# Kernel optimization log

Measured on AMD Instinct MI355X. Metric: run time of the kernel, lower is better.

The kernel has to match this reference:

```python
import jax, jax.numpy as jnp
import numpy as np

# opts hyperparameters (SCAN defaults)
LAMBDA_SOFTMAX = 9.0   # opts.lambda_softmax
LAMBDA_LSE = 6.0       # opts.lambda_lse
MARGIN = 0.2           # ContrastiveLoss margin
MAX_VIOLATION = False
NEG_INF = -1e9


def setup_inputs() -> dict:
    key = jax.random.key(0)
    k1, k2, k3 = jax.random.split(key, 3)
    I, C, R, W, D = 96, 96, 36, 48, 256  # n_image, n_recipe, n_region, max_words, dim
    images = jax.random.normal(k1, (I, R, D), dtype=jnp.float32)
    recipes = jax.random.normal(k2, (C, W, D), dtype=jnp.float32)
    # valid caption lengths in [8, W] so every caption has real words
    cap_lens = jax.random.randint(k3, (C,), 8, W + 1).astype(jnp.int32)
    return {"images": images, "recipes": recipes, "cap_lens": cap_lens}


def _xattn_score_i2t(images, recipes, cap_lens):
    """Vectorized (masked) version of the per-caption python loop.
    images: (I, R, D), recipes: (C, W, D), cap_lens: (C,) -> scores (I, C)."""
    C, W, _ = recipes.shape
    valid = jnp.arange(W)[None, :] < cap_lens[:, None]          # (C, W)
    vm = valid[:, None, :, None]                                 # (C,1,W,1)

    # raw attention: context=words (query of bmm), query=regions -> (C, I, W, R)
    attn = jnp.einsum('cwd,ird->ciwr', recipes, images)
    # clipped_l2norm: leaky_relu then l2-normalize over the word dim (dim=1 of (I,W,R))
    attn = jax.nn.leaky_relu(attn, 0.1) * vm
    nrm = jnp.sqrt(jnp.sum(attn * attn, axis=2, keepdims=True))
    attn = attn / jnp.maximum(nrm, 1e-12)

    # softmax over words with temperature lambda_softmax, masked to valid words
    logits = jnp.where(vm, attn * LAMBDA_SOFTMAX, NEG_INF)
    aw = jax.nn.softmax(logits, axis=2)                          # (C, I, W, R)

    # weighted word context per region: (C, I, R, D)
    wctx = jnp.einsum('ciwr,cwd->cird', aw, recipes)

    # cosine similarity between image regions and their attended word context
    num = jnp.einsum('cird,ird->cir', wctx, images)              # (C, I, R)
    n1 = jnp.linalg.norm(images, axis=-1)                        # (I, R)
    n2 = jnp.linalg.norm(wctx, axis=-1)                          # (C, I, R)
    row_sim = num / jnp.maximum(n1[None] * n2, 1e-8)

    # LogSumExp aggregation over regions
    sim = jax.scipy.special.logsumexp(LAMBDA_LSE * row_sim, axis=-1) / LAMBDA_LSE  # (C, I)
    return sim.T                                                  # (I, C)


def reference(images, recipes, cap_lens):
    scores = _xattn_score_i2t(images, recipes, cap_lens)          # (I, C), I == C
    B = scores.shape[0]
    diag = jnp.diagonal(scores)                                   # (B,)
    eye = jnp.eye(B, dtype=bool)
    # d2[i,j] = diag[j] (positive image score), d1[i,j] = diag[i]
    cost_image = jnp.where(eye, 0.0, jnp.maximum(MARGIN + scores - diag[None, :], 0.0))
    cost_recipe = jnp.where(eye, 0.0, jnp.maximum(MARGIN + scores - diag[:, None], 0.0))
    if MAX_VIOLATION:
        cost_image = cost_image.max(axis=0)
        cost_recipe = cost_recipe.max(axis=1)
    return cost_image.sum() + cost_recipe.sum()
```

## Files before the change

kernel.cpp:

```cpp
#include <hip/hip_runtime.h>
#include <math.h>

#define I_N 96
#define C_N 96
#define R_N 36
#define W_N 48
#define D_N 256
#define NIMG 4
#define NCOL (NIMG * R_N)
#define LAM_SM 9.0f
#define LAM_LSE 6.0f
#define MARGIN_F 0.2f
#define AWS 56

#define IMG_ELEMS (I_N * R_N * D_N)
#define REC_ELEMS (C_N * W_N * D_N)

#define WSF_SCORES 0
#define WSF_N1     9216
#define WSF_SHBASE 12800
#define SH_IMG 0
#define SH_REC IMG_ELEMS
#define SH_GP  (IMG_ELEMS + REC_ELEMS)

typedef __attribute__((ext_vector_type(8))) short short8;
typedef __attribute__((ext_vector_type(4))) float f32x4;

#define MFMA16(a, b, c) __builtin_amdgcn_mfma_f32_16x16x32_bf16(a, b, c, 0, 0, 0)

__device__ __forceinline__ unsigned short f32_to_bf16(float f) {
    unsigned int u = __float_as_uint(f);
    return (unsigned short)((u + 0x7fffu + ((u >> 16) & 1u)) >> 16);
}
__device__ __forceinline__ float dot4f(float4 a, float4 b) {
    return a.x * b.x + a.y * b.y + a.z * b.z + a.w * b.w;
}
__device__ __forceinline__ uint4 cvt8u(float4 v0, float4 v1) {
    uint4 o;
    o.x = (unsigned)f32_to_bf16(v0.x) | ((unsigned)f32_to_bf16(v0.y) << 16);
    o.y = (unsigned)f32_to_bf16(v0.z) | ((unsigned)f32_to_bf16(v0.w) << 16);
    o.z = (unsigned)f32_to_bf16(v1.x) | ((unsigned)f32_to_bf16(v1.y) << 16);
    o.w = (unsigned)f32_to_bf16(v1.z) | ((unsigned)f32_to_bf16(v1.w) << 16);
    return o;
}
__device__ __forceinline__ short8 cvt8s(float4 v0, float4 v1) {
    short8 s;
    s[0] = (short)f32_to_bf16(v0.x); s[1] = (short)f32_to_bf16(v0.y);
    s[2] = (short)f32_to_bf16(v0.z); s[3] = (short)f32_to_bf16(v0.w);
    s[4] = (short)f32_to_bf16(v1.x); s[5] = (short)f32_to_bf16(v1.y);
    s[6] = (short)f32_to_bf16(v1.z); s[7] = (short)f32_to_bf16(v1.w);
    return s;
}

__global__ __launch_bounds__(256) void prep_all(
    const float* __restrict__ images, const float* __restrict__ recipes,
    unsigned short* __restrict__ img_p, unsigned short* __restrict__ rec_p,
    unsigned short* __restrict__ Gp, float* __restrict__ n1sq)
{
    __shared__ unsigned short gt[4 * 48 * 56];
    const int bid = blockIdx.x;
    const int t = threadIdx.x;
    const int wv = t >> 6, l = t & 63;
    const int li = l & 15, q = l >> 4;

    if (bid < 72) {
        const int tile = bid / 3, chunk = bid % 3;
        const float* src = images + (size_t)tile * NCOL * D_N;
        unsigned short* dst = img_p + (size_t)tile * 72 * 512;
        #pragma unroll
        for (int ff = 0; ff < 6; ++ff) {
            int f = chunk * 24 + wv * 6 + ff;
            int rg = f >> 3, ks = f & 7;
            const float* p = src + (rg * 16 + li) * D_N + ks * 32 + q * 8;
            *(uint4*)(dst + (size_t)f * 512 + l * 8) =
                cvt8u(*(const float4*)p, *(const float4*)(p + 4));
        }
    } else if (bid < 96) {
        const int c = (bid - 72) * 4 + wv;
        const float* src = recipes + (size_t)c * W_N * D_N;
        unsigned short* rdst = rec_p + (size_t)c * 24 * 512;
        f32x4 acc[3][3];
        #pragma unroll
        for (int m = 0; m < 3; ++m)
            #pragma unroll
            for (int j = 0; j < 3; ++j) acc[m][j] = (f32x4){0.f, 0.f, 0.f, 0.f};
        #pragma unroll
        for (int ks = 0; ks < 8; ++ks) {
            short8 a[3];
            #pragma unroll
            for (int m = 0; m < 3; ++m) {
                const float* p = src + (m * 16 + li) * D_N + ks * 32 + q * 8;
                a[m] = cvt8s(*(const float4*)p, *(const float4*)(p + 4));
                *(short8*)(rdst + ((size_t)m * 8 + ks) * 512 + l * 8) = a[m];
            }
            #pragma unroll
            for (int m = 0; m < 3; ++m)
                #pragma unroll
                for (int j = 0; j < 3; ++j)
                    acc[m][j] = MFMA16(a[m], a[j], acc[m][j]);
        }
        unsigned short* g = gt + wv * 48 * 56;
        #pragma unroll
        for (int m = 0; m < 3; ++m)
            #pragma unroll
            for (int j = 0; j < 3; ++j)
                #pragma unroll
                for (int r = 0; r < 4; ++r)
                    g[(16 * m + 4 * q + r) * 56 + 16 * j + li] =
                        f32_to_bf16(acc[m][j][r]);
        asm volatile("s_waitcnt lgkmcnt(0)" ::: "memory");
        __builtin_amdgcn_sched_barrier(0);
        unsigned short* dst = Gp + (size_t)c * 3072;
        #pragma unroll
        for (int m = 0; m < 3; ++m)
            #pragma unroll
            for (int ks = 0; ks < 2; ++ks) {
                union { short8 s; uint4 u; } v;
                v.u = make_uint4(0u, 0u, 0u, 0u);
                if (32 * ks + 8 * q < 48)
                    v.s = *(const short8*)(g + (16 * m + li) * 56 + 32 * ks + 8 * q);
                *(short8*)(dst + (m * 2 + ks) * 512 + l * 8) = v.s;
            }
    } else {
        const int row = (bid - 96) * 64 + (t >> 2);
        const int sub = t & 3;
        if (row < I_N * R_N) {
            const float4* p = (const float4*)(images + (size_t)row * D_N + sub * 64);
            float s = 0.f;
            #pragma unroll
            for (int k = 0; k < 16; ++k) { float4 v = p[k]; s += dot4f(v, v); }
            s += __shfl_xor(s, 1);
            s += __shfl_xor(s, 2);
            if (sub == 0) n1sq[row] = s;
        }
    }
}

__global__ __launch_bounds__(192, 4) void xattn_main(
    const unsigned short* __restrict__ img_p, const unsigned short* __restrict__ rec_p,
    const unsigned short* __restrict__ Gp, const int* __restrict__ cap_lens,
    const float* __restrict__ n1sq, float* __restrict__ scores)
{
    __shared__ __align__(16) unsigned short ldsA[24 * 512];
    __shared__ float rs[NCOL];
    unsigned short* awL = ldsA;

    const int t = threadIdx.x;
    const int wv = t >> 6;
    const int l = t & 63;
    const int li = l & 15, q = l >> 4;
    const int sbid = ((blockIdx.x & 7) * 288) + (blockIdx.x >> 3);
    const int c = sbid % C_N;
    const int T = sbid / C_N;
    const int L = cap_lens[c];
    const int n0 = wv * 48;

    const unsigned short* pB = img_p + ((size_t)T * 72 + wv * 24) * 512 + l * 8;
    short8 bA[2][3], bB[2][3];

    #pragma unroll
    for (int kk = 0; kk < 2; ++kk)
        #pragma unroll
        for (int j = 0; j < 3; ++j)
            bA[kk][j] = *(const short8*)(pB + (j * 8 + kk) * 512);

    {
        const unsigned short* pA = rec_p + (size_t)c * 24 * 512 + l * 8;
        #pragma unroll
        for (int f0 = 0; f0 < 8; ++f0) {
            int f = wv * 8 + f0;
            *(short8*)(ldsA + f * 512 + l * 8) = *(const short8*)(pA + f * 512);
        }
    }
    __syncthreads();

    f32x4 acc[3][3];
    #pragma unroll
    for (int m = 0; m < 3; ++m)
        #pragma unroll
        for (int j = 0; j < 3; ++j) acc[m][j] = (f32x4){0.f, 0.f, 0.f, 0.f};

    #pragma unroll
    for (int kk = 0; kk < 2; ++kk)
        #pragma unroll
        for (int j = 0; j < 3; ++j)
            bB[kk][j] = *(const short8*)(pB + (j * 8 + 2 + kk) * 512);
    #pragma unroll
    for (int kk = 0; kk < 2; ++kk) {
        short8 a[3];
        #pragma unroll
        for (int m = 0; m < 3; ++m)
            a[m] = *(const short8*)(ldsA + (m * 8 + kk) * 512 + l * 8);
        #pragma unroll
        for (int m = 0; m < 3; ++m)
            #pragma unroll
            for (int j = 0; j < 3; ++j)
                acc[m][j] = MFMA16(a[m], bA[kk][j], acc[m][j]);
    }
    #pragma unroll
    for (int kk = 0; kk < 2; ++kk)
        #pragma unroll
        for (int j = 0; j < 3; ++j)
            bA[kk][j] = *(const short8*)(pB + (j * 8 + 4 + kk) * 512);
    #pragma unroll
    for (int kk = 0; kk < 2; ++kk) {
        short8 a[3];
        #pragma unroll
        for (int m = 0; m < 3; ++m)
            a[m] = *(const short8*)(ldsA + (m * 8 + 2 + kk) * 512 + l * 8);
        #pragma unroll
        for (int m = 0; m < 3; ++m)
            #pragma unroll
            for (int j = 0; j < 3; ++j)
                acc[m][j] = MFMA16(a[m], bB[kk][j], acc[m][j]);
    }
    #pragma unroll
    for (int kk = 0; kk < 2; ++kk)
        #pragma unroll
        for (int j = 0; j < 3; ++j)
            bB[kk][j] = *(const short8*)(pB + (j * 8 + 6 + kk) * 512);
    #pragma unroll
    for (int kk = 0; kk < 2; ++kk) {
        short8 a[3];
        #pragma unroll
        for (int m = 0; m < 3; ++m)
            a[m] = *(const short8*)(ldsA + (m * 8 + 4 + kk) * 512 + l * 8);
        #pragma unroll
        for (int m = 0; m < 3; ++m)
            #pragma unroll
            for (int j = 0; j < 3; ++j)
                acc[m][j] = MFMA16(a[m], bA[kk][j], acc[m][j]);
    }
    #pragma unroll
    for (int kk = 0; kk < 2; ++kk) {
        short8 a[3];
        #pragma unroll
        for (int m = 0; m < 3; ++m)
            a[m] = *(const short8*)(ldsA + (m * 8 + 6 + kk) * 512 + l * 8);
        #pragma unroll
        for (int m = 0; m < 3; ++m)
            #pragma unroll
            for (int j = 0; j < 3; ++j)
                acc[m][j] = MFMA16(a[m], bB[kk][j], acc[m][j]);
    }
    __syncthreads();

    short8 gA[3][2];
    {
        const unsigned short* pg = Gp + (size_t)c * 3072 + l * 8;
        #pragma unroll
        for (int m = 0; m < 3; ++m)
            #pragma unroll
            for (int ks = 0; ks < 2; ++ks)
                gA[m][ks] = *(const short8*)(pg + (m * 2 + ks) * 512);
    }
    float n1v[3];
    #pragma unroll
    for (int j = 0; j < 3; ++j)
        n1v[j] = n1sq[T * NCOL + n0 + 16 * j + li];

    float nume[3];
    #pragma unroll
    for (int j = 0; j < 3; ++j) {
        const int n = n0 + 16 * j + li;
        float v[3][4];
        float ssq = 0.f;
        #pragma unroll
        for (int m = 0; m < 3; ++m)
            #pragma unroll
            for (int r = 0; r < 4; ++r) {
                int w = 16 * m + 4 * q + r;
                float x = acc[m][j][r];
                float lv = fmaxf(x, 0.1f * x);
                float lm = (w < L) ? lv : 0.f;
                v[m][r] = lm;
                ssq = fmaf(lm, lm, ssq);
            }
        ssq += __shfl_xor(ssq, 16); ssq += __shfl_xor(ssq, 32);
        float inv = LAM_SM * rsqrtf(fmaxf(ssq, 1e-24f));
        float np = 0.f;
        #pragma unroll
        for (int m = 0; m < 3; ++m) {
            int w0 = 16 * m + 4 * q;
            float e0 = (w0     < L) ? __expf(v[m][0] * inv) : 0.f;
            float e1 = (w0 + 1 < L) ? __expf(v[m][1] * inv) : 0.f;
            float e2 = (w0 + 2 < L) ? __expf(v[m][2] * inv) : 0.f;
            float e3 = (w0 + 3 < L) ? __expf(v[m][3] * inv) : 0.f;
            np = fmaf(e0, acc[m][j][0], np);
            np = fmaf(e1, acc[m][j][1], np);
            np = fmaf(e2, acc[m][j][2], np);
            np = fmaf(e3, acc[m][j][3], np);
            unsigned lo, hi;
            asm("v_cvt_pk_bf16_f32 %0, %1, %2" : "=v"(lo) : "v"(e0), "v"(e1));
            asm("v_cvt_pk_bf16_f32 %0, %1, %2" : "=v"(hi) : "v"(e2), "v"(e3));
            *(uint2*)(awL + n * AWS + 16 * m + 4 * q) = make_uint2(lo, hi);
        }
        np += __shfl_xor(np, 16); np += __shfl_xor(np, 32);
        nume[j] = np;
    }
    asm volatile("s_waitcnt lgkmcnt(0)" ::: "memory");
    __builtin_amdgcn_sched_barrier(0);

    #pragma unroll
    for (int m = 0; m < 3; ++m)
        #pragma unroll
        for (int j = 0; j < 3; ++j) acc[m][j] = (f32x4){0.f, 0.f, 0.f, 0.f};
    #pragma unroll
    for (int ks = 0; ks < 2; ++ks) {
        short8 b[3];
        #pragma unroll
        for (int j = 0; j < 3; ++j) {
            union { short8 s; uint4 u; } bv;
            bv.u = make_uint4(0u, 0u, 0u, 0u);
            if (32 * ks + 8 * q < 48) {
                const uint2* p =
                    (const uint2*)(awL + (n0 + 16 * j + li) * AWS + 32 * ks + 8 * q);
                uint2 x0 = p[0], x1 = p[1];
                bv.u = make_uint4(x0.x, x0.y, x1.x, x1.y);
            }
            b[j] = bv.s;
        }
        #pragma unroll
        for (int m = 0; m < 3; ++m)
            #pragma unroll
            for (int j = 0; j < 3; ++j)
                acc[m][j] = MFMA16(gA[m][ks], b[j], acc[m][j]);
    }

    #pragma unroll
    for (int j = 0; j < 3; ++j) {
        const int n = n0 + 16 * j + li;
        const unsigned short* ap = awL + n * AWS + 4 * q;
        float n2p = 0.f;
        #pragma unroll
        for (int m = 0; m < 3; ++m) {
            uint2 u = *(const uint2*)(ap + 16 * m);
            n2p = fmaf(__uint_as_float(u.x << 16),          acc[m][j][0], n2p);
            n2p = fmaf(__uint_as_float(u.x & 0xffff0000u),  acc[m][j][1], n2p);
            n2p = fmaf(__uint_as_float(u.y << 16),          acc[m][j][2], n2p);
            n2p = fmaf(__uint_as_float(u.y & 0xffff0000u),  acc[m][j][3], n2p);
        }
        n2p += __shfl_xor(n2p, 16); n2p += __shfl_xor(n2p, 32);
        if (q == 0)
            rs[n] = nume[j] * rsqrtf(fmaxf(n1v[j] * n2p, 1e-16f));
    }
    __syncthreads();

    if (t < 32) {
        int ii = t >> 3, k = t & 7;
        float mx = -1e30f;
        #pragma unroll
        for (int p = 0; p < 5; ++p) {
            int r = k + 8 * p;
            if (r < R_N) mx = fmaxf(mx, rs[ii * R_N + r]);
        }
        mx = fmaxf(mx, __shfl_xor(mx, 1));
        mx = fmaxf(mx, __shfl_xor(mx, 2));
        mx = fmaxf(mx, __shfl_xor(mx, 4));
        float s = 0.f;
        #pragma unroll
        for (int p = 0; p < 5; ++p) {
            int r = k + 8 * p;
            if (r < R_N) s += __expf(LAM_LSE * (rs[ii * R_N + r] - mx));
        }
        s += __shfl_xor(s, 1); s += __shfl_xor(s, 2); s += __shfl_xor(s, 4);
        if (k == 0)
            scores[(size_t)(T * NIMG + ii) * C_N + c] =
                (LAM_LSE * mx + __logf(s)) / LAM_LSE;
    }
}

__global__ __launch_bounds__(1024) void hinge_loss_kernel(
    const float* __restrict__ S, float* __restrict__ out)
{
    __shared__ float diag[96];
    __shared__ float wsum[16];
    const int t = threadIdx.x;
    if (t < 96) diag[t] = S[t * 97];
    __syncthreads();
    float acc = 0.f;
    #pragma unroll
    for (int p = 0; p < 9; ++p) {
        int k = t + 1024 * p;
        if (k < C_N * C_N) {
            int ii = k / 96;
            int cc = k - ii * 96;
            if (ii != cc) {
                float s = S[k];
                acc += fmaxf(MARGIN_F + s - diag[cc], 0.f)
                     + fmaxf(MARGIN_F + s - diag[ii], 0.f);
            }
        }
    }
    #pragma unroll
    for (int off = 32; off; off >>= 1) acc += __shfl_xor(acc, off);
    if ((t & 63) == 0) wsum[t >> 6] = acc;
    __syncthreads();
    if (t == 0) {
        float s = 0.f;
        #pragma unroll
        for (int w = 0; w < 16; ++w) s += wsum[w];
        out[0] = s;
    }
}

extern "C" void kernel_launch(void* const* d_in, const int* in_sizes, int n_in,
                              void* d_out, int out_size, void* d_ws, size_t ws_size,
                              hipStream_t stream) {
    const float* images  = (const float*)d_in[0];
    const float* recipes = (const float*)d_in[1];
    const int*   caps    = (const int*)d_in[2];
    float* out = (float*)d_out;
    float* wsf = (float*)d_ws;
    float* scores = wsf + WSF_SCORES;
    float* n1 = wsf + WSF_N1;
    unsigned short* shb = (unsigned short*)(wsf + WSF_SHBASE);
    unsigned short* img_p = shb + SH_IMG;
    unsigned short* rec_p = shb + SH_REC;
    unsigned short* Gpp   = shb + SH_GP;

    hipLaunchKernelGGL(prep_all, dim3(150), dim3(256), 0, stream,
                       images, recipes, img_p, rec_p, Gpp, n1);
    hipLaunchKernelGGL(xattn_main, dim3(2304), dim3(192), 0, stream,
                       img_p, rec_p, Gpp, caps, n1, scores);
    hipLaunchKernelGGL(hinge_loss_kernel, dim3(1), dim3(1024), 0, stream, scores, out);
}
```

Measured before the change: 39.03 us.

## Process three image tiles per block, reusing recipe LDS and softmax-context operands

Each block of xattn_main now loops over three image tiles for a given caption, so the grid shrinks from 2304 to 768 blocks. The recipe tile is loaded into LDS once, along with the G operand registers, and reused across the three tiles. A separate LDS buffer holds the attention weights, so the next tile's image fragments can be prefetched while the current tile's softmax runs. In exchange it uses more LDS per block, lowers the occupancy hint from 4 to 3, serializes work within a block, and leaves fewer blocks to spread across the CUs.

```diff
diff --git a/kernel.cpp b/kernel.cpp
--- a/kernel.cpp
+++ b/kernel.cpp
@@ -136,115 +136,44 @@
     }
 }
 
-__global__ __launch_bounds__(192, 4) void xattn_main(
+__global__ __launch_bounds__(192, 3) void xattn_main(
     const unsigned short* __restrict__ img_p, const unsigned short* __restrict__ rec_p,
     const unsigned short* __restrict__ Gp, const int* __restrict__ cap_lens,
     const float* __restrict__ n1sq, float* __restrict__ scores)
 {
-    __shared__ __align__(16) unsigned short ldsA[24 * 512];
+    __shared__ __align__(16) unsigned short recL[24 * 512];
+    __shared__ __align__(16) unsigned short awL[NCOL * AWS];
     __shared__ float rs[NCOL];
-    unsigned short* awL = ldsA;
 
     const int t = threadIdx.x;
     const int wv = t >> 6;
     const int l = t & 63;
     const int li = l & 15, q = l >> 4;
-    const int sbid = ((blockIdx.x & 7) * 288) + (blockIdx.x >> 3);
+    const int sbid = ((blockIdx.x & 7) * 96) + (blockIdx.x >> 3);
     const int c = sbid % C_N;
-    const int T = sbid / C_N;
+    const int tg = sbid / C_N;
     const int L = cap_lens[c];
     const int n0 = wv * 48;
 
-    const unsigned short* pB = img_p + ((size_t)T * 72 + wv * 24) * 512 + l * 8;
     short8 bA[2][3], bB[2][3];
 
-    #pragma unroll
-    for (int kk = 0; kk < 2; ++kk)
-        #pragma unroll
-        for (int j = 0; j < 3; ++j)
-            bA[kk][j] = *(const short8*)(pB + (j * 8 + kk) * 512);
-
+    {
+        const unsigned short* pB0 =
+            img_p + ((size_t)(3 * tg) * 72 + wv * 24) * 512 + l * 8;
+        #pragma unroll
+        for (int kk = 0; kk < 2; ++kk)
+            #pragma unroll
+            for (int j = 0; j < 3; ++j)
+                bA[kk][j] = *(const short8*)(pB0 + (j * 8 + kk) * 512);
+    }
     {
         const unsigned short* pA = rec_p + (size_t)c * 24 * 512 + l * 8;
         #pragma unroll
         for (int f0 = 0; f0 < 8; ++f0) {
             int f = wv * 8 + f0;
-            *(short8*)(ldsA + f * 512 + l * 8) = *(const short8*)(pA + f * 512);
-        }
-    }
-    __syncthreads();
-
-    f32x4 acc[3][3];
-    #pragma unroll
-    for (int m = 0; m < 3; ++m)
-        #pragma unroll
-        for (int j = 0; j < 3; ++j) acc[m][j] = (f32x4){0.f, 0.f, 0.f, 0.f};
-
-    #pragma unroll
-    for (int kk = 0; kk < 2; ++kk)
-        #pragma unroll
-        for (int j = 0; j < 3; ++j)
-            bB[kk][j] = *(const short8*)(pB + (j * 8 + 2 + kk) * 512);
-    #pragma unroll
-    for (int kk = 0; kk < 2; ++kk) {
-        short8 a[3];
-        #pragma unroll
-        for (int m = 0; m < 3; ++m)
-            a[m] = *(const short8*)(ldsA + (m * 8 + kk) * 512 + l * 8);
-        #pragma unroll
-        for (int m = 0; m < 3; ++m)
-            #pragma unroll
-            for (int j = 0; j < 3; ++j)
-                acc[m][j] = MFMA16(a[m], bA[kk][j], acc[m][j]);
-    }
-    #pragma unroll
-    for (int kk = 0; kk < 2; ++kk)
-        #pragma unroll
-        for (int j = 0; j < 3; ++j)
-            bA[kk][j] = *(const short8*)(pB + (j * 8 + 4 + kk) * 512);
-    #pragma unroll
-    for (int kk = 0; kk < 2; ++kk) {
-        short8 a[3];
-        #pragma unroll
-        for (int m = 0; m < 3; ++m)
-            a[m] = *(const short8*)(ldsA + (m * 8 + 2 + kk) * 512 + l * 8);
-        #pragma unroll
-        for (int m = 0; m < 3; ++m)
-            #pragma unroll
-            for (int j = 0; j < 3; ++j)
-                acc[m][j] = MFMA16(a[m], bB[kk][j], acc[m][j]);
-    }
-    #pragma unroll
-    for (int kk = 0; kk < 2; ++kk)
-        #pragma unroll
-        for (int j = 0; j < 3; ++j)
-            bB[kk][j] = *(const short8*)(pB + (j * 8 + 6 + kk) * 512);
-    #pragma unroll
-    for (int kk = 0; kk < 2; ++kk) {
-        short8 a[3];
-        #pragma unroll
-        for (int m = 0; m < 3; ++m)
-            a[m] = *(const short8*)(ldsA + (m * 8 + 4 + kk) * 512 + l * 8);
-        #pragma unroll
-        for (int m = 0; m < 3; ++m)
-            #pragma unroll
-            for (int j = 0; j < 3; ++j)
-                acc[m][j] = MFMA16(a[m], bA[kk][j], acc[m][j]);
-    }
-    #pragma unroll
-    for (int kk = 0; kk < 2; ++kk) {
-        short8 a[3];
-        #pragma unroll
-        for (int m = 0; m < 3; ++m)
-            a[m] = *(const short8*)(ldsA + (m * 8 + 6 + kk) * 512 + l * 8);
-        #pragma unroll
-        for (int m = 0; m < 3; ++m)
-            #pragma unroll
-            for (int j = 0; j < 3; ++j)
-                acc[m][j] = MFMA16(a[m], bB[kk][j], acc[m][j]);
-    }
-    __syncthreads();
-
+            *(short8*)(recL + f * 512 + l * 8) = *(const short8*)(pA + f * 512);
+        }
+    }
     short8 gA[3][2];
     {
         const unsigned short* pg = Gp + (size_t)c * 3072 + l * 8;
@@ -254,119 +183,207 @@
             for (int ks = 0; ks < 2; ++ks)
                 gA[m][ks] = *(const short8*)(pg + (m * 2 + ks) * 512);
     }
-    float n1v[3];
-    #pragma unroll
-    for (int j = 0; j < 3; ++j)
-        n1v[j] = n1sq[T * NCOL + n0 + 16 * j + li];
-
-    float nume[3];
-    #pragma unroll
-    for (int j = 0; j < 3; ++j) {
-        const int n = n0 + 16 * j + li;
-        float v[3][4];
-        float ssq = 0.f;
-        #pragma unroll
-        for (int m = 0; m < 3; ++m)
-            #pragma unroll
-            for (int r = 0; r < 4; ++r) {
-                int w = 16 * m + 4 * q + r;
-                float x = acc[m][j][r];
-                float lv = fmaxf(x, 0.1f * x);
-                float lm = (w < L) ? lv : 0.f;
-                v[m][r] = lm;
-                ssq = fmaf(lm, lm, ssq);
-            }
-        ssq += __shfl_xor(ssq, 16); ssq += __shfl_xor(ssq, 32);
-        float inv = LAM_SM * rsqrtf(fmaxf(ssq, 1e-24f));
-        float np = 0.f;
-        #pragma unroll
-        for (int m = 0; m < 3; ++m) {
-            int w0 = 16 * m + 4 * q;
-            float e0 = (w0     < L) ? __expf(v[m][0] * inv) : 0.f;
-            float e1 = (w0 + 1 < L) ? __expf(v[m][1] * inv) : 0.f;
-            float e2 = (w0 + 2 < L) ? __expf(v[m][2] * inv) : 0.f;
-            float e3 = (w0 + 3 < L) ? __expf(v[m][3] * inv) : 0.f;
-            np = fmaf(e0, acc[m][j][0], np);
-            np = fmaf(e1, acc[m][j][1], np);
-            np = fmaf(e2, acc[m][j][2], np);
-            np = fmaf(e3, acc[m][j][3], np);
-            unsigned lo, hi;
-            asm("v_cvt_pk_bf16_f32 %0, %1, %2" : "=v"(lo) : "v"(e0), "v"(e1));
-            asm("v_cvt_pk_bf16_f32 %0, %1, %2" : "=v"(hi) : "v"(e2), "v"(e3));
-            *(uint2*)(awL + n * AWS + 16 * m + 4 * q) = make_uint2(lo, hi);
-        }
-        np += __shfl_xor(np, 16); np += __shfl_xor(np, 32);
-        nume[j] = np;
-    }
-    asm volatile("s_waitcnt lgkmcnt(0)" ::: "memory");
-    __builtin_amdgcn_sched_barrier(0);
-
-    #pragma unroll
-    for (int m = 0; m < 3; ++m)
-        #pragma unroll
-        for (int j = 0; j < 3; ++j) acc[m][j] = (f32x4){0.f, 0.f, 0.f, 0.f};
-    #pragma unroll
-    for (int ks = 0; ks < 2; ++ks) {
-        short8 b[3];
+    __syncthreads();
+
+    for (int tt = 0; tt < 3; ++tt) {
+        const int T = 3 * tg + tt;
+        const unsigned short* pB = img_p + ((size_t)T * 72 + wv * 24) * 512 + l * 8;
+
+        f32x4 acc[3][3];
+        #pragma unroll
+        for (int m = 0; m < 3; ++m)
+            #pragma unroll
+            for (int j = 0; j < 3; ++j) acc[m][j] = (f32x4){0.f, 0.f, 0.f, 0.f};
+
+        #pragma unroll
+        for (int kk = 0; kk < 2; ++kk)
+            #pragma unroll
+            for (int j = 0; j < 3; ++j)
+                bB[kk][j] = *(const short8*)(pB + (j * 8 + 2 + kk) * 512);
+        #pragma unroll
+        for (int kk = 0; kk < 2; ++kk) {
+            short8 a[3];
+            #pragma unroll
+            for (int m = 0; m < 3; ++m)
+                a[m] = *(const short8*)(recL + (m * 8 + kk) * 512 + l * 8);
+            #pragma unroll
+            for (int m = 0; m < 3; ++m)
+                #pragma unroll
+                for (int j = 0; j < 3; ++j)
+                    acc[m][j] = MFMA16(a[m], bA[kk][j], acc[m][j]);
+        }
+        #pragma unroll
+        for (int kk = 0; kk < 2; ++kk)
+            #pragma unroll
+            for (int j = 0; j < 3; ++j)
+                bA[kk][j] = *(const short8*)(pB + (j * 8 + 4 + kk) * 512);
+        #pragma unroll
+        for (int kk = 0; kk < 2; ++kk) {
+            short8 a[3];
+            #pragma unroll
+            for (int m = 0; m < 3; ++m)
+                a[m] = *(const short8*)(recL + (m * 8 + 2 + kk) * 512 + l * 8);
+            #pragma unroll
+            for (int m = 0; m < 3; ++m)
+                #pragma unroll
+                for (int j = 0; j < 3; ++j)
+                    acc[m][j] = MFMA16(a[m], bB[kk][j], acc[m][j]);
+        }
+        #pragma unroll
+        for (int kk = 0; kk < 2; ++kk)
+            #pragma unroll
+            for (int j = 0; j < 3; ++j)
+                bB[kk][j] = *(const short8*)(pB + (j * 8 + 6 + kk) * 512);
+        #pragma unroll
+        for (int kk = 0; kk < 2; ++kk) {
+            short8 a[3];
+            #pragma unroll
+            for (int m = 0; m < 3; ++m)
+                a[m] = *(const short8*)(recL + (m * 8 + 4 + kk) * 512 + l * 8);
+            #pragma unroll
+            for (int m = 0; m < 3; ++m)
+                #pragma unroll
+                for (int j = 0; j < 3; ++j)
+                    acc[m][j] = MFMA16(a[m], bA[kk][j], acc[m][j]);
+        }
+        #pragma unroll
+        for (int kk = 0; kk < 2; ++kk) {
+            short8 a[3];
+            #pragma unroll
+            for (int m = 0; m < 3; ++m)
+                a[m] = *(const short8*)(recL + (m * 8 + 6 + kk) * 512 + l * 8);
+            #pragma unroll
+            for (int m = 0; m < 3; ++m)
+                #pragma unroll
+                for (int j = 0; j < 3; ++j)
+                    acc[m][j] = MFMA16(a[m], bB[kk][j], acc[m][j]);
+        }
+
+        __syncthreads();
+
+        if (tt < 2) {
+            const unsigned short* pBn =
+                img_p + ((size_t)(T + 1) * 72 + wv * 24) * 512 + l * 8;
+            #pragma unroll
+            for (int kk = 0; kk < 2; ++kk)
+                #pragma unroll
+                for (int j = 0; j < 3; ++j)
+                    bA[kk][j] = *(const short8*)(pBn + (j * 8 + kk) * 512);
+        }
+        float n1v[3];
+        #pragma unroll
+        for (int j = 0; j < 3; ++j)
+            n1v[j] = n1sq[T * NCOL + n0 + 16 * j + li];
+
+        float nume[3];
         #pragma unroll
         for (int j = 0; j < 3; ++j) {
-            union { short8 s; uint4 u; } bv;
-            bv.u = make_uint4(0u, 0u, 0u, 0u);
-            if (32 * ks + 8 * q < 48) {
-                const uint2* p =
-                    (const uint2*)(awL + (n0 + 16 * j + li) * AWS + 32 * ks + 8 * q);
-                uint2 x0 = p[0], x1 = p[1];
-                bv.u = make_uint4(x0.x, x0.y, x1.x, x1.y);
-            }
-            b[j] = bv.s;
-        }
-        #pragma unroll
-        for (int m = 0; m < 3; ++m)
-            #pragma unroll
-            for (int j = 0; j < 3; ++j)
-                acc[m][j] = MFMA16(gA[m][ks], b[j], acc[m][j]);
-    }
-
-    #pragma unroll
-    for (int j = 0; j < 3; ++j) {
-        const int n = n0 + 16 * j + li;
-        const unsigned short* ap = awL + n * AWS + 4 * q;
-        float n2p = 0.f;
-        #pragma unroll
-        for (int m = 0; m < 3; ++m) {
-            uint2 u = *(const uint2*)(ap + 16 * m);
-            n2p = fmaf(__uint_as_float(u.x << 16),          acc[m][j][0], n2p);
-            n2p = fmaf(__uint_as_float(u.x & 0xffff0000u),  acc[m][j][1], n2p);
-            n2p = fmaf(__uint_as_float(u.y << 16),          acc[m][j][2], n2p);
-            n2p = fmaf(__uint_as_float(u.y & 0xffff0000u),  acc[m][j][3], n2p);
-        }
-        n2p += __shfl_xor(n2p, 16); n2p += __shfl_xor(n2p, 32);
-        if (q == 0)
-            rs[n] = nume[j] * rsqrtf(fmaxf(n1v[j] * n2p, 1e-16f));
-    }
-    __syncthreads();
-
-    if (t < 32) {
-        int ii = t >> 3, k = t & 7;
-        float mx = -1e30f;
-        #pragma unroll
-        for (int p = 0; p < 5; ++p) {
-            int r = k + 8 * p;
-            if (r < R_N) mx = fmaxf(mx, rs[ii * R_N + r]);
-        }
-        mx = fmaxf(mx, __shfl_xor(mx, 1));
-        mx = fmaxf(mx, __shfl_xor(mx, 2));
-        mx = fmaxf(mx, __shfl_xor(mx, 4));
-        float s = 0.f;
-        #pragma unroll
-        for (int p = 0; p < 5; ++p) {
-            int r = k + 8 * p;
-            if (r < R_N) s += __expf(LAM_LSE * (rs[ii * R_N + r] - mx));
-        }
-        s += __shfl_xor(s, 1); s += __shfl_xor(s, 2); s += __shfl_xor(s, 4);
-        if (k == 0)
-            scores[(size_t)(T * NIMG + ii) * C_N + c] =
-                (LAM_LSE * mx + __logf(s)) / LAM_LSE;
+            const int n = n0 + 16 * j + li;
+            float v[3][4];
+            float ssq = 0.f;
+            #pragma unroll
+            for (int m = 0; m < 3; ++m)
+                #pragma unroll
+                for (int r = 0; r < 4; ++r) {
+                    int w = 16 * m + 4 * q + r;
+                    float x = acc[m][j][r];
+                    float lv = fmaxf(x, 0.1f * x);
+                    float lm = (w < L) ? lv : 0.f;
+                    v[m][r] = lm;
+                    ssq = fmaf(lm, lm, ssq);
+                }
+            ssq += __shfl_xor(ssq, 16); ssq += __shfl_xor(ssq, 32);
+            float inv = LAM_SM * rsqrtf(fmaxf(ssq, 1e-24f));
+            float np = 0.f;
+            #pragma unroll
+            for (int m = 0; m < 3; ++m) {
+                int w0 = 16 * m + 4 * q;
+                float e0 = (w0     < L) ? __expf(v[m][0] * inv) : 0.f;
+                float e1 = (w0 + 1 < L) ? __expf(v[m][1] * inv) : 0.f;
+                float e2 = (w0 + 2 < L) ? __expf(v[m][2] * inv) : 0.f;
+                float e3 = (w0 + 3 < L) ? __expf(v[m][3] * inv) : 0.f;
+                np = fmaf(e0, acc[m][j][0], np);
+                np = fmaf(e1, acc[m][j][1], np);
+                np = fmaf(e2, acc[m][j][2], np);
+                np = fmaf(e3, acc[m][j][3], np);
+                unsigned lo, hi;
+                asm("v_cvt_pk_bf16_f32 %0, %1, %2" : "=v"(lo) : "v"(e0), "v"(e1));
+                asm("v_cvt_pk_bf16_f32 %0, %1, %2" : "=v"(hi) : "v"(e2), "v"(e3));
+                *(uint2*)(awL + n * AWS + 16 * m + 4 * q) = make_uint2(lo, hi);
+            }
+            np += __shfl_xor(np, 16); np += __shfl_xor(np, 32);
+            nume[j] = np;
+        }
+        asm volatile("s_waitcnt lgkmcnt(0)" ::: "memory");
+        __builtin_amdgcn_sched_barrier(0);
+
+        #pragma unroll
+        for (int m = 0; m < 3; ++m)
+            #pragma unroll
+            for (int j = 0; j < 3; ++j) acc[m][j] = (f32x4){0.f, 0.f, 0.f, 0.f};
+        #pragma unroll
+        for (int ks = 0; ks < 2; ++ks) {
+            short8 b[3];
+            #pragma unroll
+            for (int j = 0; j < 3; ++j) {
+                union { short8 s; uint4 u; } bv;
+                bv.u = make_uint4(0u, 0u, 0u, 0u);
+                if (32 * ks + 8 * q < 48) {
+                    const uint2* p =
+                        (const uint2*)(awL + (n0 + 16 * j + li) * AWS + 32 * ks + 8 * q);
+                    uint2 x0 = p[0], x1 = p[1];
+                    bv.u = make_uint4(x0.x, x0.y, x1.x, x1.y);
+                }
+                b[j] = bv.s;
+            }
+            #pragma unroll
+            for (int m = 0; m < 3; ++m)
+                #pragma unroll
+                for (int j = 0; j < 3; ++j)
+                    acc[m][j] = MFMA16(gA[m][ks], b[j], acc[m][j]);
+        }
+
+        #pragma unroll
+        for (int j = 0; j < 3; ++j) {
+            const int n = n0 + 16 * j + li;
+            const unsigned short* ap = awL + n * AWS + 4 * q;
+            float n2p = 0.f;
+            #pragma unroll
+            for (int m = 0; m < 3; ++m) {
+                uint2 u = *(const uint2*)(ap + 16 * m);
+                n2p = fmaf(__uint_as_float(u.x << 16),          acc[m][j][0], n2p);
+                n2p = fmaf(__uint_as_float(u.x & 0xffff0000u),  acc[m][j][1], n2p);
+                n2p = fmaf(__uint_as_float(u.y << 16),          acc[m][j][2], n2p);
+                n2p = fmaf(__uint_as_float(u.y & 0xffff0000u),  acc[m][j][3], n2p);
+            }
+            n2p += __shfl_xor(n2p, 16); n2p += __shfl_xor(n2p, 32);
+            if (q == 0)
+                rs[n] = nume[j] * rsqrtf(fmaxf(n1v[j] * n2p, 1e-16f));
+        }
+        __syncthreads();
+
+        if (t < 32) {
+            int ii = t >> 3, k = t & 7;
+            float mx = -1e30f;
+            #pragma unroll
+            for (int p = 0; p < 5; ++p) {
+                int r = k + 8 * p;
+                if (r < R_N) mx = fmaxf(mx, rs[ii * R_N + r]);
+            }
+            mx = fmaxf(mx, __shfl_xor(mx, 1));
+            mx = fmaxf(mx, __shfl_xor(mx, 2));
+            mx = fmaxf(mx, __shfl_xor(mx, 4));
+            float s = 0.f;
+            #pragma unroll
+            for (int p = 0; p < 5; ++p) {
+                int r = k + 8 * p;
+                if (r < R_N) s += __expf(LAM_LSE * (rs[ii * R_N + r] - mx));
+            }
+            s += __shfl_xor(s, 1); s += __shfl_xor(s, 2); s += __shfl_xor(s, 4);
+            if (k == 0)
+                scores[(size_t)(T * NIMG + ii) * C_N + c] =
+                    (LAM_LSE * mx + __logf(s)) / LAM_LSE;
+        }
     }
 }
 
@@ -421,7 +438,7 @@
 
     hipLaunchKernelGGL(prep_all, dim3(150), dim3(256), 0, stream,
                        images, recipes, img_p, rec_p, Gpp, n1);
-    hipLaunchKernelGGL(xattn_main, dim3(2304), dim3(192), 0, stream,
+    hipLaunchKernelGGL(xattn_main, dim3(768), dim3(192), 0, stream,
                        img_p, rec_p, Gpp, caps, n1, scores);
     hipLaunchKernelGGL(hinge_loss_kernel, dim3(1), dim3(1024), 0, stream, scores, out);
 }
```

Measured after the change: 40.83 us. 1.05x slower.
